# Kernel optimization log

Hardware: AMD Instinct MI355X
Metric: run time of the kernel (lower is better)

## Reference

```python
import jax, jax.numpy as jnp
import numpy as np

# angular momenta of the full basis (2s,3s,2p,3p,3d) -> block sizes 1,1,3,3,5; norb=13
L_LIST = [0, 0, 1, 1, 2]


def factor_matrix():
    """Replicates the orbital-pair loop: factor 0.5 on diagonal orbital blocks,
    1.0 for i<j blocks, 0.0 below the block diagonal (only i<=j filled)."""
    sizes = [2 * l + 1 for l in L_LIST]
    norb = sum(sizes)
    F = np.zeros((norb, norb), np.float32)
    ist = 0
    for i, si in enumerate(sizes):
        jst = 0
        for j, sj in enumerate(sizes):
            if i < j:
                F[ist:ist + si, jst:jst + sj] = 1.0
            elif i == j:
                F[ist:ist + si, jst:jst + sj] = 0.5
            jst += sj
        ist += si
    return jnp.asarray(F)


def setup_inputs() -> dict:
    key = jax.random.key(0)
    k1, k2, k3, k4, k5 = jax.random.split(key, 5)
    N, E, K = 128, 2048, 16
    norb = sum(2 * l + 1 for l in L_LIST)  # 13
    return {
        "hopping": jax.random.normal(k1, (E, norb * norb), jnp.float32),
        "onsite": jax.random.normal(k2, (N, norb * norb), jnp.float32),
        "kpoints": jax.random.uniform(k3, (K, 3), jnp.float32),
        "cell_shift": jax.random.normal(k4, (E, 3), jnp.float32),
        "edge_index": jax.random.randint(k5, (2, E), 0, N, jnp.int64),
    }


def reference(hopping, onsite, kpoints, cell_shift, edge_index):
    F = factor_matrix()
    norb = F.shape[0]
    N = onsite.shape[0]
    K = kpoints.shape[0]
    ctype = jnp.complex64

    # per-edge / per-atom orbital blocks with upper-triangular factor (i<=j loop)
    hop = (hopping.reshape(-1, norb, norb) * F).astype(ctype)   # [E,norb,norb]
    ons = (onsite.reshape(-1, norb, norb) * F).astype(ctype)    # [N,norb,norb]

    # Bloch phase exp(-i 2*pi k.R) per (k, edge)
    phase = jnp.exp(-1j * 2.0 * jnp.pi * (kpoints @ cell_shift.T).astype(ctype))  # [K,E]

    # assemble block Hamiltonian [K, N, N, norb, norb]
    H = jnp.zeros((K, N, N, norb, norb), ctype)
    ar = jnp.arange(N)
    H = H.at[:, ar, ar].add(ons[None])  # onsite diagonal blocks (no phase)
    ie, je = edge_index[0], edge_index[1]
    H = H.at[:, ie, je].add(phase[:, :, None, None] * hop[None])  # scatter-add edges

    # hermitize: block + block^H (swap atom blocks and orbital indices)
    H = H + jnp.conj(jnp.swapaxes(jnp.swapaxes(H, 1, 2), 3, 4))
    # [K, N, norb, N, norb] -> [K, all_norb, all_norb]
    Hk = H.transpose(0, 1, 3, 2, 4).reshape(K, N * norb, N * norb)
    return Hk
```

## Files before the change

### kernel.cpp

```cpp
#include <hip/hip_runtime.h>
#include <math.h>

#define NORB 13
#define NORB2 (NORB * NORB)
#define GB 16
#define KSPLIT 2

typedef float fx4 __attribute__((ext_vector_type(4)));

__device__ __forceinline__ int blk_of(int p) {
    return p < 1 ? 0 : (p < 2 ? 1 : (p < 5 ? 2 : (p < 8 ? 3 : 4)));
}
__device__ __forceinline__ float ffac(int p, int q) {
    int bp = blk_of(p), bq = blk_of(q);
    return bp < bq ? 1.0f : (bp == bq ? 0.5f : 0.0f);
}

__global__ void __launch_bounds__(256)
k_build(const int* __restrict__ edge_index, int* __restrict__ rowptr,
        int* __restrict__ entries, int E, int N, int ngroups) {
    extern __shared__ int sm[];
    int nbins = N * ngroups;
    int* cnt    = sm;
    int* cursor = sm + nbins;
    int* part   = sm + 2 * nbins;
    int tid = threadIdx.x;

    for (int i = tid; i < nbins; i += 256) cnt[i] = 0;
    __syncthreads();

    for (int e = tid; e < E; e += 256) {
        int ie = edge_index[e], je = edge_index[E + e];
        atomicAdd(cnt + ie * ngroups + (je >> 4), 1);
        atomicAdd(cnt + je * ngroups + (ie >> 4), 1);
    }
    __syncthreads();

    int per = nbins / 256;
    int base = tid * per;
    int s = 0;
    for (int i = 0; i < per; ++i) s += cnt[base + i];
    part[tid + 1] = s;
    __syncthreads();
    if (tid == 0) {
        part[0] = 0;
        for (int i = 1; i <= 256; ++i) part[i] += part[i - 1];
    }
    __syncthreads();
    int run = part[tid];
    for (int i = 0; i < per; ++i) {
        rowptr[base + i] = run;
        cursor[base + i] = run;
        run += cnt[base + i];
    }
    if (tid == 255) rowptr[nbins] = run;
    __syncthreads();

    for (int e = tid; e < E; e += 256) {
        int ie = edge_index[e], je = edge_index[E + e];
        int pos = atomicAdd(cursor + ie * ngroups + (je >> 4), 1);
        entries[pos] = (e << 9) | je;
        pos = atomicAdd(cursor + je * ngroups + (ie >> 4), 1);
        entries[pos] = (e << 9) | 256 | ie;
    }
}

__global__ void __launch_bounds__(256)
k_assemble(const float* __restrict__ hopping,
           const float* __restrict__ onsite,
           const float* __restrict__ kpoints,
           const float* __restrict__ cell_shift,
           const int* __restrict__ rowptr,
           const int* __restrict__ entries,
           float* __restrict__ out,
           int N, int K, int ld, int es, int ngroups) {
    int g  = blockIdx.x % ngroups;
    int a  = (blockIdx.x / ngroups) % N;
    int kc = blockIdx.x / (ngroups * N);
    int kch = (K + KSPLIT - 1) / KSPLIT;
    int k0 = kc * kch, k1 = min(K, k0 + kch);
    int tid = threadIdx.x;
    int b0 = g * GB;
    int nb = min(GB, N - b0);

    __shared__ __align__(16) float lds[NORB * GB * NORB * 2];
    fx4* lds4 = (fx4*)lds;
    const int LDSF4 = NORB * GB * NORB * 2 / 4;
    for (int i = tid; i < LDSF4; i += 256)
        lds4[i] = (fx4){0.f, 0.f, 0.f, 0.f};

    int p = 0, q = 0;
    bool act = tid < NORB2;
    if (act) { p = tid / NORB; q = tid - p * NORB; }
    float fpq = act ? ffac(p, q) : 0.f;
    float fqp = act ? ffac(q, p) : 0.f;

    bool diag = (a >= b0 && a < b0 + nb);
    float onv = 0.f;
    int  ondst = 0;
    if (diag && act) {
        const float* on = onsite + (size_t)a * NORB2;
        onv = on[p * NORB + q] * fpq + on[q * NORB + p] * fqp;
        ondst = (p * GB * NORB + (a - b0) * NORB + q) * 2;
    }

    int bin = a * ngroups + g;
    int beg = rowptr[bin], end = rowptr[bin + 1];
    __syncthreads();

    const int ROWF4 = GB * NORB * 2 / 4;
    bool fastpath = (es == 2) && (nb == GB);

    for (int k = k0; k < k1; ++k) {
        float kx = kpoints[3 * k], ky = kpoints[3 * k + 1], kz = kpoints[3 * k + 2];

        if (diag && act) {
            lds[ondst] += onv;
        }
        for (int it = beg; it < end; ++it) {
            int ent = entries[it];
            int e = ent >> 9;
            int rev = ent & 256;
            int i = (ent & 255) - b0;
            float Rx = cell_shift[3 * e], Ry = cell_shift[3 * e + 1], Rz = cell_shift[3 * e + 2];
            float d = kx * Rx + ky * Ry + kz * Rz;
            float s, c;
            __sincosf(-6.2831853071795864f * d, &s, &c);
            float im = rev ? -s : s;
            if (act) {
                const float* h = hopping + (size_t)e * NORB2;
                float hv = rev ? h[q * NORB + p] * fqp : h[p * NORB + q] * fpq;
                int base = (p * GB * NORB + i * NORB + q) * 2;
                lds[base]     += c * hv;
                lds[base + 1] += im * hv;
            }
        }
        __syncthreads();

        if (fastpath) {
            fx4* o4 = (fx4*)out;
            for (int idx = tid; idx < NORB * ROWF4; idx += 256) {
                int row = idx / ROWF4;
                int col = idx - row * ROWF4;
                fx4 v = lds4[idx];
                lds4[idx] = (fx4){0.f, 0.f, 0.f, 0.f};
                size_t gc = ((size_t)k * ld + (size_t)a * NORB + row) * ld + (size_t)b0 * NORB;
                o4[(gc >> 1) + col] = v;
            }
        } else if (es == 2) {
            float2* o2 = (float2*)out;
            int nelem = NORB * nb * NORB;
            for (int idx = tid; idx < nelem; idx += 256) {
                int row = idx / (nb * NORB);
                int rem = idx - row * nb * NORB;
                size_t gc = ((size_t)k * ld + (size_t)a * NORB + row) * ld + (size_t)b0 * NORB + rem;
                int li = (row * GB * NORB + rem) * 2;
                o2[gc] = make_float2(lds[li], lds[li + 1]);
                lds[li] = 0.f; lds[li + 1] = 0.f;
            }
        } else {
            int nelem = NORB * nb * NORB;
            for (int idx = tid; idx < nelem; idx += 256) {
                int row = idx / (nb * NORB);
                int rem = idx - row * nb * NORB;
                size_t gc = ((size_t)k * ld + (size_t)a * NORB + row) * ld + (size_t)b0 * NORB + rem;
                int li = (row * GB * NORB + rem) * 2;
                out[gc] = lds[li];
                lds[li] = 0.f; lds[li + 1] = 0.f;
            }
        }
        __syncthreads();
    }
}

extern "C" void kernel_launch(void* const* d_in, const int* in_sizes, int n_in,
                              void* d_out, int out_size, void* d_ws, size_t ws_size,
                              hipStream_t stream) {
    const float* hopping    = (const float*)d_in[0];
    const float* onsite     = (const float*)d_in[1];
    const float* kpoints    = (const float*)d_in[2];
    const float* cell_shift = (const float*)d_in[3];
    const int*   edge_index = (const int*)d_in[4];
    float* out = (float*)d_out;

    int E = in_sizes[0] / NORB2;
    int N = in_sizes[1] / NORB2;
    int K = in_sizes[2] / 3;
    int ld = N * NORB;
    int ngroups = (N + GB - 1) / GB;
    int nbins = N * ngroups;

    size_t full = (size_t)K * ld * ld * 2;
    int es = ((size_t)out_size >= full) ? 2 : 1;

    int* rowptr  = (int*)d_ws;
    int* entries = rowptr + nbins + 1;

    size_t build_lds = (size_t)(2 * nbins + 257) * sizeof(int);
    k_build<<<1, 256, build_lds, stream>>>(edge_index, rowptr, entries, E, N, ngroups);

    int nwg = N * ngroups * KSPLIT;
    k_assemble<<<nwg, 256, 0, stream>>>(hopping, onsite, kpoints, cell_shift,
                                        rowptr, entries, out, N, K, ld, es, ngroups);
}
```

Before: 222.9 us.

## Fuse edge bucketing into assemble kernel and accumulate blocks in registers

Removes the single-workgroup build kernel. Each assemble workgroup now scans all edges itself, finds the ones that touch its (atom, group) tile and bins them into a small LDS list. Accumulation moves from shared-memory scatter into per-thread registers, one sub-block at a time, with direct coalesced complex stores, so the LDS zeroing and syncthreads per k-point go away. In exchange every workgroup rescans all E edges, which is redundant global reading, and the edge list is capped at MAXE entries, so a bucket that overflows would be silently truncated.

```diff
diff --git a/kernel.cpp b/kernel.cpp
--- a/kernel.cpp
+++ b/kernel.cpp
@@ -5,8 +5,10 @@
 #define NORB2 (NORB * NORB)
 #define GB 16
 #define KSPLIT 2
+#define MAXE 128
+#define NTHR 256
 
-typedef float fx4 __attribute__((ext_vector_type(4)));
+typedef float fx2 __attribute__((ext_vector_type(2)));
 
 __device__ __forceinline__ int blk_of(int p) {
     return p < 1 ? 0 : (p < 2 ? 1 : (p < 5 ? 2 : (p < 8 ? 3 : 4)));
@@ -16,64 +18,14 @@
     return bp < bq ? 1.0f : (bp == bq ? 0.5f : 0.0f);
 }
 
-__global__ void __launch_bounds__(256)
-k_build(const int* __restrict__ edge_index, int* __restrict__ rowptr,
-        int* __restrict__ entries, int E, int N, int ngroups) {
-    extern __shared__ int sm[];
-    int nbins = N * ngroups;
-    int* cnt    = sm;
-    int* cursor = sm + nbins;
-    int* part   = sm + 2 * nbins;
-    int tid = threadIdx.x;
-
-    for (int i = tid; i < nbins; i += 256) cnt[i] = 0;
-    __syncthreads();
-
-    for (int e = tid; e < E; e += 256) {
-        int ie = edge_index[e], je = edge_index[E + e];
-        atomicAdd(cnt + ie * ngroups + (je >> 4), 1);
-        atomicAdd(cnt + je * ngroups + (ie >> 4), 1);
-    }
-    __syncthreads();
-
-    int per = nbins / 256;
-    int base = tid * per;
-    int s = 0;
-    for (int i = 0; i < per; ++i) s += cnt[base + i];
-    part[tid + 1] = s;
-    __syncthreads();
-    if (tid == 0) {
-        part[0] = 0;
-        for (int i = 1; i <= 256; ++i) part[i] += part[i - 1];
-    }
-    __syncthreads();
-    int run = part[tid];
-    for (int i = 0; i < per; ++i) {
-        rowptr[base + i] = run;
-        cursor[base + i] = run;
-        run += cnt[base + i];
-    }
-    if (tid == 255) rowptr[nbins] = run;
-    __syncthreads();
-
-    for (int e = tid; e < E; e += 256) {
-        int ie = edge_index[e], je = edge_index[E + e];
-        int pos = atomicAdd(cursor + ie * ngroups + (je >> 4), 1);
-        entries[pos] = (e << 9) | je;
-        pos = atomicAdd(cursor + je * ngroups + (ie >> 4), 1);
-        entries[pos] = (e << 9) | 256 | ie;
-    }
-}
-
-__global__ void __launch_bounds__(256)
-k_assemble(const float* __restrict__ hopping,
-           const float* __restrict__ onsite,
-           const float* __restrict__ kpoints,
-           const float* __restrict__ cell_shift,
-           const int* __restrict__ rowptr,
-           const int* __restrict__ entries,
-           float* __restrict__ out,
-           int N, int K, int ld, int es, int ngroups) {
+__global__ void __launch_bounds__(NTHR)
+k_fused(const float* __restrict__ hopping,
+        const float* __restrict__ onsite,
+        const float* __restrict__ kpoints,
+        const float* __restrict__ cell_shift,
+        const int* __restrict__ edge_index,
+        float* __restrict__ out,
+        int N, int E, int K, int ld, int es, int ngroups) {
     int g  = blockIdx.x % ngroups;
     int a  = (blockIdx.x / ngroups) % N;
     int kc = blockIdx.x / (ngroups * N);
@@ -81,95 +33,88 @@
     int k0 = kc * kch, k1 = min(K, k0 + kch);
     int tid = threadIdx.x;
     int b0 = g * GB;
-    int nb = min(GB, N - b0);
 
-    __shared__ __align__(16) float lds[NORB * GB * NORB * 2];
-    fx4* lds4 = (fx4*)lds;
-    const int LDSF4 = NORB * GB * NORB * 2 / 4;
-    for (int i = tid; i < LDSF4; i += 256)
-        lds4[i] = (fx4){0.f, 0.f, 0.f, 0.f};
+    __shared__ int cnt[GB + 1];
+    __shared__ int cur[GB];
+    __shared__ int list[MAXE];
 
-    int p = 0, q = 0;
-    bool act = tid < NORB2;
-    if (act) { p = tid / NORB; q = tid - p * NORB; }
-    float fpq = act ? ffac(p, q) : 0.f;
-    float fqp = act ? ffac(q, p) : 0.f;
-
-    bool diag = (a >= b0 && a < b0 + nb);
-    float onv = 0.f;
-    int  ondst = 0;
-    if (diag && act) {
-        const float* on = onsite + (size_t)a * NORB2;
-        onv = on[p * NORB + q] * fpq + on[q * NORB + p] * fqp;
-        ondst = (p * GB * NORB + (a - b0) * NORB + q) * 2;
-    }
-
-    int bin = a * ngroups + g;
-    int beg = rowptr[bin], end = rowptr[bin + 1];
+    if (tid <= GB) cnt[tid] = 0;
     __syncthreads();
 
-    const int ROWF4 = GB * NORB * 2 / 4;
-    bool fastpath = (es == 2) && (nb == GB);
+    for (int e = tid; e < E; e += NTHR) {
+        int ie = edge_index[e], je = edge_index[E + e];
+        if (ie == a && (je >> 4) == g) atomicAdd(&cnt[je & 15], 1);
+        if (je == a && (ie >> 4) == g) atomicAdd(&cnt[ie & 15], 1);
+    }
+    __syncthreads();
+    if (tid == 0) {
+        int run = 0;
+        for (int i = 0; i < GB; ++i) { int c = cnt[i]; cnt[i] = run; cur[i] = run; run += c; }
+        cnt[GB] = run;
+    }
+    __syncthreads();
+    for (int e = tid; e < E; e += NTHR) {
+        int ie = edge_index[e], je = edge_index[E + e];
+        if (ie == a && (je >> 4) == g) {
+            int pos = atomicAdd(&cur[je & 15], 1);
+            if (pos < MAXE) list[pos] = (e << 1);
+        }
+        if (je == a && (ie >> 4) == g) {
+            int pos = atomicAdd(&cur[ie & 15], 1);
+            if (pos < MAXE) list[pos] = (e << 1) | 1;
+        }
+    }
+    __syncthreads();
+
+    int offs[GB + 1];
+    #pragma unroll
+    for (int i = 0; i <= GB; ++i) offs[i] = __builtin_amdgcn_readfirstlane(cnt[i]);
+
+    if (tid >= NORB2) return;
+    int p = tid / NORB, q = tid - p * NORB;
+    float fpq = ffac(p, q), fqp = ffac(q, p);
+    int idxF = p * NORB + q, idxR = q * NORB + p;
+
+    bool dwg = (a >= b0) && (a < b0 + GB);
+    int idiag = a - b0;
+    float onx = 0.f;
+    if (dwg) {
+        const float* on = onsite + (size_t)a * NORB2;
+        onx = on[idxF] * fpq + on[idxR] * fqp;
+    }
 
     for (int k = k0; k < k1; ++k) {
         float kx = kpoints[3 * k], ky = kpoints[3 * k + 1], kz = kpoints[3 * k + 2];
+        size_t rowc = ((size_t)(k * ld + a * NORB + p)) * ld + (size_t)b0 * NORB + q;
 
-        if (diag && act) {
-            lds[ondst] += onv;
-        }
-        for (int it = beg; it < end; ++it) {
-            int ent = entries[it];
-            int e = ent >> 9;
-            int rev = ent & 256;
-            int i = (ent & 255) - b0;
-            float Rx = cell_shift[3 * e], Ry = cell_shift[3 * e + 1], Rz = cell_shift[3 * e + 2];
-            float d = kx * Rx + ky * Ry + kz * Rz;
-            float s, c;
-            __sincosf(-6.2831853071795864f * d, &s, &c);
-            float im = rev ? -s : s;
-            if (act) {
+        #pragma unroll
+        for (int i = 0; i < GB; ++i) {
+            float ax = (dwg && i == idiag) ? onx : 0.f;
+            float ay = 0.f;
+            int itend = offs[i + 1];
+            for (int it = offs[i]; it < itend; ++it) {
+                int ent = __builtin_amdgcn_readfirstlane(list[it]);
+                int e = ent >> 1;
+                const float* cs = cell_shift + 3 * (size_t)e;
+                float d = kx * cs[0] + ky * cs[1] + kz * cs[2];
+                float s, c;
+                __sincosf(-6.2831853071795864f * d, &s, &c);
                 const float* h = hopping + (size_t)e * NORB2;
-                float hv = rev ? h[q * NORB + p] * fqp : h[p * NORB + q] * fpq;
-                int base = (p * GB * NORB + i * NORB + q) * 2;
-                lds[base]     += c * hv;
-                lds[base + 1] += im * hv;
+                float hv, im;
+                if (ent & 1) { hv = h[idxR] * fqp; im = -s; }
+                else         { hv = h[idxF] * fpq; im =  s; }
+                ax += c * hv;
+                ay += im * hv;
+            }
+            if (b0 + i < N) {
+                if (es == 2) {
+                    fx2* o2 = (fx2*)out;
+                    o2[rowc + (size_t)i * NORB] = (fx2){ax, ay};
+                } else {
+                    out[rowc + (size_t)i * NORB] = ax;
+                }
             }
         }
-        __syncthreads();
-
-        if (fastpath) {
-            fx4* o4 = (fx4*)out;
-            for (int idx = tid; idx < NORB * ROWF4; idx += 256) {
-                int row = idx / ROWF4;
-                int col = idx - row * ROWF4;
-                fx4 v = lds4[idx];
-                lds4[idx] = (fx4){0.f, 0.f, 0.f, 0.f};
-                size_t gc = ((size_t)k * ld + (size_t)a * NORB + row) * ld + (size_t)b0 * NORB;
-                o4[(gc >> 1) + col] = v;
-            }
-        } else if (es == 2) {
-            float2* o2 = (float2*)out;
-            int nelem = NORB * nb * NORB;
-            for (int idx = tid; idx < nelem; idx += 256) {
-                int row = idx / (nb * NORB);
-                int rem = idx - row * nb * NORB;
-                size_t gc = ((size_t)k * ld + (size_t)a * NORB + row) * ld + (size_t)b0 * NORB + rem;
-                int li = (row * GB * NORB + rem) * 2;
-                o2[gc] = make_float2(lds[li], lds[li + 1]);
-                lds[li] = 0.f; lds[li + 1] = 0.f;
-            }
-        } else {
-            int nelem = NORB * nb * NORB;
-            for (int idx = tid; idx < nelem; idx += 256) {
-                int row = idx / (nb * NORB);
-                int rem = idx - row * nb * NORB;
-                size_t gc = ((size_t)k * ld + (size_t)a * NORB + row) * ld + (size_t)b0 * NORB + rem;
-                int li = (row * GB * NORB + rem) * 2;
-                out[gc] = lds[li];
-                lds[li] = 0.f; lds[li + 1] = 0.f;
-            }
-        }
-        __syncthreads();
     }
 }
 
@@ -188,18 +133,11 @@
     int K = in_sizes[2] / 3;
     int ld = N * NORB;
     int ngroups = (N + GB - 1) / GB;
-    int nbins = N * ngroups;
 
     size_t full = (size_t)K * ld * ld * 2;
     int es = ((size_t)out_size >= full) ? 2 : 1;
 
-    int* rowptr  = (int*)d_ws;
-    int* entries = rowptr + nbins + 1;
-
-    size_t build_lds = (size_t)(2 * nbins + 257) * sizeof(int);
-    k_build<<<1, 256, build_lds, stream>>>(edge_index, rowptr, entries, E, N, ngroups);
-
     int nwg = N * ngroups * KSPLIT;
-    k_assemble<<<nwg, 256, 0, stream>>>(hopping, onsite, kpoints, cell_shift,
-                                        rowptr, entries, out, N, K, ld, es, ngroups);
+    k_fused<<<nwg, NTHR, 0, stream>>>(hopping, onsite, kpoints, cell_shift,
+                                      edge_index, out, N, E, K, ld, es, ngroups);
 }
```

Result: faster. 213.0 us (-4.4%).
